# Kernel tuning notes

Measured on AMD Instinct MI355X. Metric: run time of the kernel, lower is better.

Reference implementation:

```python
import math
import jax, jax.numpy as jnp
import numpy as np

N_HEADS = 8
GROUPS = 32
EPS = 1e-5


def setup_inputs() -> dict:
    key = jax.random.key(0)
    ks = jax.random.split(key, 4)
    B, C, H, W = 8, 512, 32, 32
    x = jax.random.normal(ks[0], (B, C, H, W), dtype=jnp.float32)
    gn_scale = jnp.ones((C,), dtype=jnp.float32)
    gn_bias = jnp.zeros((C,), dtype=jnp.float32)
    # small init so softmax logits stay in a sane range (original zero-inits
    # proj_out; we use small random weights so the output is non-trivial)
    qkv_w = jax.random.normal(ks[1], (3 * C, C), dtype=jnp.float32) * 0.02
    qkv_b = jnp.zeros((3 * C,), dtype=jnp.float32)
    proj_w = jax.random.normal(ks[2], (C, C), dtype=jnp.float32) * 0.02
    proj_b = jnp.zeros((C,), dtype=jnp.float32)
    return {"x": x, "gn_scale": gn_scale, "gn_bias": gn_bias,
            "qkv_w": qkv_w, "qkv_b": qkv_b,
            "proj_w": proj_w, "proj_b": proj_b}


def reference(x, gn_scale, gn_bias, qkv_w, qkv_b, proj_w, proj_b):
    b, c, H, W = x.shape
    L = H * W
    xr = x.reshape(b, c, L)

    # GroupNorm32: normalize in fp32 over (channels_per_group, L)
    xf = xr.astype(jnp.float32).reshape(b, GROUPS, -1)
    mu = xf.mean(axis=-1, keepdims=True)
    var = xf.var(axis=-1, keepdims=True)
    xn = ((xf - mu) * jax.lax.rsqrt(var + EPS)).reshape(b, c, L)
    xn = (xn * gn_scale[:, None] + gn_bias[:, None]).astype(x.dtype)

    # 1x1 conv QKV projection: [b, 3C, L]
    qkv = jnp.einsum('oc,bcl->bol', qkv_w, xn) + qkv_b[:, None]

    # QKVAttentionLegacy: split 3C axis as (heads, 3*ch)
    ch = c // N_HEADS
    qkv = qkv.reshape(b * N_HEADS, 3 * ch, L)
    q, k, v = qkv[:, :ch], qkv[:, ch:2 * ch], qkv[:, 2 * ch:]
    scale = 1.0 / math.sqrt(math.sqrt(ch))
    w = jnp.einsum('bct,bcs->bts', q * scale, k * scale)  # [b*h, L, L]
    w = jax.nn.softmax(w.astype(jnp.float32), axis=-1).astype(qkv.dtype)
    a = jnp.einsum('bts,bcs->bct', w, v).reshape(b, c, L)

    # 1x1 conv output projection + residual
    h = jnp.einsum('oc,bcl->bol', proj_w, a) + proj_b[:, None]
    return (xr + h).reshape(b, c, H, W)
```

## Files before the change

kernel.cpp:

```cpp
#include <hip/hip_runtime.h>
#include <hip/hip_bf16.h>

typedef __attribute__((ext_vector_type(8))) short v8s;
typedef __attribute__((ext_vector_type(4))) short v4s;
typedef __attribute__((ext_vector_type(8))) unsigned short u16x8;
typedef __attribute__((ext_vector_type(4))) float v4f;

#define MFMA16(a, b, c) __builtin_amdgcn_mfma_f32_16x16x32_bf16((a), (b), (c), 0, 0, 0)

#if __has_builtin(__builtin_amdgcn_mfma_f32_16x16x16_bf16)
#define MFMA16K16(a, b, c) __builtin_amdgcn_mfma_f32_16x16x16_bf16((a), (b), (c), 0, 0, 0)
#elif __has_builtin(__builtin_amdgcn_mfma_f32_16x16x16bf16_1k)
#define MFMA16K16(a, b, c) __builtin_amdgcn_mfma_f32_16x16x16bf16_1k((a), (b), (c), 0, 0, 0)
#else
static __device__ __forceinline__ v4f mfma16k16_asm(v4s a, v4s b, v4f c) {
  v4f d;
  asm("v_mfma_f32_16x16x16_bf16 %0, %1, %2, %3" : "=v"(d) : "v"(a), "v"(b), "v"(c));
  return d;
}
#define MFMA16K16(a, b, c) mfma16k16_asm((a), (b), (c))
#endif

#define GLL16(g, l)                                                        \
  __builtin_amdgcn_global_load_lds(                                        \
      (const __attribute__((address_space(1))) unsigned int*)(g),          \
      (__attribute__((address_space(3))) unsigned int*)(l), 16, 0, 0)

#if __has_builtin(__builtin_amdgcn_exp2f)
__device__ __forceinline__ float exp2n(float x) { return __builtin_amdgcn_exp2f(x); }
#else
__device__ __forceinline__ float exp2n(float x) {
  float r; asm("v_exp_f32 %0, %1" : "=v"(r) : "v"(x)); return r;
}
#endif

__device__ __forceinline__ unsigned short f2bf(float f) {
  union { float f; unsigned u; } v; v.f = f;
  unsigned r = v.u + 0x7fffu + ((v.u >> 16) & 1u);
  return (unsigned short)(r >> 16);
}
__device__ __forceinline__ unsigned packbf2(float lo, float hi) {
  union { float f; unsigned u; } a, b; a.f = lo; b.f = hi;
  return (a.u >> 16) | (b.u & 0xffff0000u);
}

__global__ __launch_bounds__(256) void cvt_gn_kernel(const float* __restrict__ in0,
                                                     unsigned short* __restrict__ out0,
                                                     const float* __restrict__ in1,
                                                     unsigned short* __restrict__ out1,
                                                     int n0, int n1,
                                                     const float* __restrict__ x,
                                                     float2* __restrict__ stats) {
  if (blockIdx.x < 1024) {
    int i = blockIdx.x * 256 + threadIdx.x;
    const float* in; unsigned short* out;
    if (i < n0) { in = in0; out = out0; }
    else        { i -= n0; if (i >= n1) return; in = in1; out = out1; }
    float4 v = ((const float4*)in)[i];
    ushort4 o;
    o.x = f2bf(v.x); o.y = f2bf(v.y); o.z = f2bf(v.z); o.w = f2bf(v.w);
    ((ushort4*)out)[i] = o;
    return;
  }
  const int bg = blockIdx.x - 1024;
  const float4* xp4 = (const float4*)(x + (size_t)bg * 16 * 1024);
  float s = 0.f, ss = 0.f;
  for (int i = threadIdx.x; i < 4096; i += 256) {
    float4 v = xp4[i];
    s  += (v.x + v.y) + (v.z + v.w);
    ss += (v.x * v.x + v.y * v.y) + (v.z * v.z + v.w * v.w);
  }
  #pragma unroll
  for (int d = 1; d < 64; d <<= 1) { s += __shfl_xor(s, d); ss += __shfl_xor(ss, d); }
  __shared__ float red[2][4];
  const int w = threadIdx.x >> 6;
  if ((threadIdx.x & 63) == 0) { red[0][w] = s; red[1][w] = ss; }
  __syncthreads();
  if (threadIdx.x == 0) {
    s  = red[0][0] + red[0][1] + red[0][2] + red[0][3];
    ss = red[1][0] + red[1][1] + red[1][2] + red[1][3];
    const float mu  = s * (1.f / 16384.f);
    const float var = ss * (1.f / 16384.f) - mu * mu;
    stats[bg] = make_float2(mu, rsqrtf(var + 1e-5f));
  }
}

__global__ __launch_bounds__(256) void gnt_kernel(const float* __restrict__ x,
                                                  const float2* __restrict__ stats,
                                                  const float* __restrict__ gsc,
                                                  const float* __restrict__ gbi,
                                                  unsigned short* __restrict__ xnT) {
  const int b = blockIdx.z, l0 = blockIdx.x * 64, c0 = blockIdx.y * 64;
  const float* sp = x + (size_t)b * 512 * 1024;
  unsigned short* dp = xnT + (size_t)b * 1024 * 512;
  __shared__ unsigned T[64][65];
  const int tid = threadIdx.x;
  const int rr = tid >> 3, c8 = (tid & 7) * 8;
  #pragma unroll
  for (int sw = 0; sw < 2; ++sw) {
    const int c = c0 + sw * 32 + rr;
    const float2 st = stats[b * 32 + (c >> 4)];
    const float sc = gsc[c] * st.y;
    const float bi = gbi[c] - st.x * sc;
    const float4* px = (const float4*)(sp + (size_t)c * 1024 + l0 + c8);
    float4 v0 = px[0], v1 = px[1];
    T[sw * 32 + rr][c8 + 0] = f2bf(v0.x * sc + bi);
    T[sw * 32 + rr][c8 + 1] = f2bf(v0.y * sc + bi);
    T[sw * 32 + rr][c8 + 2] = f2bf(v0.z * sc + bi);
    T[sw * 32 + rr][c8 + 3] = f2bf(v0.w * sc + bi);
    T[sw * 32 + rr][c8 + 4] = f2bf(v1.x * sc + bi);
    T[sw * 32 + rr][c8 + 5] = f2bf(v1.y * sc + bi);
    T[sw * 32 + rr][c8 + 6] = f2bf(v1.z * sc + bi);
    T[sw * 32 + rr][c8 + 7] = f2bf(v1.w * sc + bi);
  }
  __syncthreads();
  #pragma unroll
  for (int sw = 0; sw < 2; ++sw) {
    const int ll = sw * 32 + rr;
    u16x8 o;
    #pragma unroll
    for (int j = 0; j < 8; ++j) o[j] = (unsigned short)T[c8 + j][ll];
    *(u16x8*)(dp + (size_t)(l0 + ll) * 512 + c0 + c8) = o;
  }
}

template <bool QKV, int NT>
__global__ __launch_bounds__(256) void gemm_kernel(
    const unsigned short* __restrict__ A,
    const unsigned short* __restrict__ BT,
    const float* __restrict__ bias,
    const float* __restrict__ xres,
    float* __restrict__ outf,
    unsigned short* __restrict__ qT,
    unsigned short* __restrict__ kT,
    unsigned short* __restrict__ vO) {
  constexpr int K = 512;
  constexpr int NFR = NT / 32;
  constexpr int NJOB = 16 + NT / 8;
  const int n0 = blockIdx.x * NT, m0 = blockIdx.y * 128, b = blockIdx.z;
  const unsigned short* Bp = BT + (size_t)b * 1024 * K;

  __shared__ __align__(16) unsigned short As[128][64];
  __shared__ __align__(16) unsigned short Bs[NT][64];

  const int tid = threadIdx.x, lane = tid & 63, w = tid >> 6;
  const int quad = lane >> 4, l15 = lane & 15;
  const int wm = (w >> 1) * 64, wn = (w & 1) * (NT / 2);
  const int srow = lane >> 3;
  const int scol = ((lane & 7) ^ srow) * 8;
  const int ck0 = ((quad ^ (l15 & 7)) * 8);
  const int ck1 = ck0 ^ 32;
  const unsigned short* Asf = &As[0][0];
  const unsigned short* Bsf = &Bs[0][0];

  v4f acc[4][NFR];
  #pragma unroll
  for (int i = 0; i < 4; ++i)
    #pragma unroll
    for (int j = 0; j < NFR; ++j) acc[i][j] = (v4f){0.f, 0.f, 0.f, 0.f};

  for (int kk = 0; kk < K; kk += 64) {
    __syncthreads();
    #pragma unroll
    for (int jj = 0; jj < NJOB / 4; ++jj) {
      const int job = w * (NJOB / 4) + jj;
      if (job < 16) {
        GLL16(A + (size_t)(m0 + job * 8 + srow) * K + kk + scol, &As[job * 8][0]);
      } else {
        const int j2 = job - 16;
        GLL16(Bp + (size_t)(n0 + j2 * 8 + srow) * K + kk + scol, &Bs[j2 * 8][0]);
      }
    }
    __syncthreads();
    #pragma unroll
    for (int h = 0; h < 2; ++h) {
      const int ck = h ? ck1 : ck0;
      v8s af[4], bf[NFR];
      #pragma unroll
      for (int mt = 0; mt < 4; ++mt) af[mt] = *(const v8s*)(Asf + (wm + mt * 16 + l15) * 64 + ck);
      #pragma unroll
      for (int nt = 0; nt < NFR; ++nt) bf[nt] = *(const v8s*)(Bsf + (wn + nt * 16 + l15) * 64 + ck);
      #pragma unroll
      for (int mt = 0; mt < 4; ++mt)
        #pragma unroll
        for (int nt = 0; nt < NFR; ++nt)
          acc[mt][nt] = MFMA16(af[mt], bf[nt], acc[mt][nt]);
    }
  }

  if (QKV) {
    const int bh8 = b * 8;
    const float cs = 0.18033688011112042f;
    #pragma unroll
    for (int mt = 0; mt < 4; ++mt) {
      const int m4 = m0 + wm + mt * 16 + quad * 4;
      const int h = m4 / 192;
      const int rr = m4 - h * 192;
      const int part = rr >> 6;
      const int ch = rr & 63;
      const float b0 = bias[m4], b1 = bias[m4 + 1], b2 = bias[m4 + 2], b3 = bias[m4 + 3];
      #pragma unroll
      for (int nt = 0; nt < NFR; ++nt) {
        const int n = n0 + wn + nt * 16 + l15;
        v4f a = acc[mt][nt];
        const float v0 = a[0] + b0, v1 = a[1] + b1, v2 = a[2] + b2, v3 = a[3] + b3;
        if (part == 0) {
          ushort4 st4;
          st4.x = f2bf(v0 * cs); st4.y = f2bf(v1 * cs);
          st4.z = f2bf(v2 * cs); st4.w = f2bf(v3 * cs);
          *(ushort4*)(qT + ((size_t)(bh8 + h) * 1024 + n) * 64 + ch) = st4;
        } else if (part == 1) {
          ushort4 st4;
          st4.x = f2bf(v0); st4.y = f2bf(v1); st4.z = f2bf(v2); st4.w = f2bf(v3);
          *(ushort4*)(kT + ((size_t)(bh8 + h) * 1024 + n) * 64 + ch) = st4;
        } else {
          unsigned short* dp = vO + ((size_t)(bh8 + h) * 64 + ch) * 1024 + n;
          dp[0] = f2bf(v0); dp[1024] = f2bf(v1); dp[2048] = f2bf(v2); dp[3072] = f2bf(v3);
        }
      }
    }
  } else {
    #pragma unroll
    for (int mt = 0; mt < 4; ++mt) {
      const int m4 = m0 + wm + mt * 16 + quad * 4;
      const float b0 = bias[m4], b1 = bias[m4 + 1], b2 = bias[m4 + 2], b3 = bias[m4 + 3];
      #pragma unroll
      for (int nt = 0; nt < NFR; ++nt) {
        const int n = n0 + wn + nt * 16 + l15;
        const size_t i0 = ((size_t)b * 512 + m4) * 1024 + n;
        outf[i0]        = xres[i0]        + acc[mt][nt][0] + b0;
        outf[i0 + 1024] = xres[i0 + 1024] + acc[mt][nt][1] + b1;
        outf[i0 + 2048] = xres[i0 + 2048] + acc[mt][nt][2] + b2;
        outf[i0 + 3072] = xres[i0 + 3072] + acc[mt][nt][3] + b3;
      }
    }
  }
}

__global__ __launch_bounds__(256) void attn_kernel(const unsigned short* __restrict__ qT,
                                                   const unsigned short* __restrict__ kT,
                                                   const unsigned short* __restrict__ vv,
                                                   unsigned short* __restrict__ aT) {
  const int bh = blockIdx.x;
  const int t0 = blockIdx.y * 128;
  const unsigned short* qb = qT + (size_t)bh * 1024 * 64;
  const unsigned short* kb = kT + (size_t)bh * 1024 * 64;
  const unsigned short* vb = vv + (size_t)bh * 64 * 1024;

  __shared__ __align__(16) unsigned short Ks[2][128][64];
  __shared__ __align__(16) unsigned short Vs[2][2][64][64];

  const int tid = threadIdx.x, w = tid >> 6, lane = tid & 63;
  const int quad = lane >> 4, l15 = lane & 15;
  const int srow = lane >> 3;
  const int scol = ((lane & 7) ^ srow) * 8;
  const int ck0 = ((quad ^ (l15 & 7)) * 8);
  const int ck1 = ck0 ^ 32;

  #pragma unroll
  for (int jj = 0; jj < 4; ++jj) {
    const int seg = w * 4 + jj;
    GLL16(qb + (size_t)(t0 + seg * 8 + srow) * 64 + scol, &Ks[0][seg * 8][0]);
  }
  __syncthreads();
  v8s qf[2][2];
  #pragma unroll
  for (int tg = 0; tg < 2; ++tg) {
    qf[tg][0] = *(const v8s*)(&Ks[0][0][0] + (w * 32 + tg * 16 + l15) * 64 + ck0);
    qf[tg][1] = *(const v8s*)(&Ks[0][0][0] + (w * 32 + tg * 16 + l15) * 64 + ck1);
  }
  __syncthreads();

  #pragma unroll
  for (int jj = 0; jj < 8; ++jj) {
    const int j = w * 8 + jj;
    if (j < 16) {
      GLL16(kb + (size_t)(j * 8 + srow) * 64 + scol, &Ks[0][j * 8][0]);
    } else {
      const int j2 = j - 16, hf = j2 >> 3, cg = (j2 & 7) * 8;
      GLL16(vb + (size_t)(cg + srow) * 1024 + hf * 64 + scol, &Vs[0][hf][cg][0]);
    }
  }

  v4f o[2][4];
  #pragma unroll
  for (int tg = 0; tg < 2; ++tg)
    #pragma unroll
    for (int i = 0; i < 4; ++i) o[tg][i] = (v4f){0.f, 0.f, 0.f, 0.f};
  float lsum[2] = {0.f, 0.f};

  const int vq4 = (quad & 1) * 4;
  const int vqh = quad >> 1;

  for (int it = 0; it < 8; ++it) {
    __syncthreads();
    if (it + 1 < 8) {
      const int s1 = (it + 1) * 128, bp1 = (it + 1) & 1;
      #pragma unroll
      for (int jj = 0; jj < 8; ++jj) {
        const int j = w * 8 + jj;
        if (j < 16) {
          GLL16(kb + (size_t)(s1 + j * 8 + srow) * 64 + scol, &Ks[bp1][j * 8][0]);
        } else {
          const int j2 = j - 16, hf = j2 >> 3, cg = (j2 & 7) * 8;
          GLL16(vb + (size_t)(cg + srow) * 1024 + s1 + hf * 64 + scol,
                &Vs[bp1][hf][cg][0]);
        }
      }
    }
    const int buf = it & 1;

    #pragma unroll
    for (int hf = 0; hf < 2; ++hf) {
      const unsigned short* Kb = &Ks[buf][hf * 64][0];
      const unsigned short* Vb = &Vs[buf][hf][0][0];

      v4f sa[2][4];
      #pragma unroll
      for (int st = 0; st < 4; ++st) {
        v8s k0 = *(const v8s*)(Kb + (st * 16 + l15) * 64 + ck0);
        v8s k1 = *(const v8s*)(Kb + (st * 16 + l15) * 64 + ck1);
        #pragma unroll
        for (int tg = 0; tg < 2; ++tg) {
          v4f z = (v4f){0.f, 0.f, 0.f, 0.f};
          z = MFMA16(k0, qf[tg][0], z);
          sa[tg][st] = MFMA16(k1, qf[tg][1], z);
        }
      }

      union { v4s v; unsigned u[2]; } pa[2][4];
      #pragma unroll
      for (int tg = 0; tg < 2; ++tg) {
        float rsum = 0.f;
        #pragma unroll
        for (int st = 0; st < 4; ++st) {
          float p0 = exp2n(sa[tg][st][0]);
          float p1 = exp2n(sa[tg][st][1]);
          float p2 = exp2n(sa[tg][st][2]);
          float p3 = exp2n(sa[tg][st][3]);
          rsum += (p0 + p1) + (p2 + p3);
          pa[tg][st].u[0] = packbf2(p0, p1);
          pa[tg][st].u[1] = packbf2(p2, p3);
        }
        lsum[tg] += rsum;
      }

      #pragma unroll
      for (int nc = 0; nc < 4; ++nc) {
        const int row = nc * 16 + l15;
        const unsigned short* vrow = Vb + row * 64 + vq4;
        const int rx = row & 7;
        #pragma unroll
        for (int st = 0; st < 4; ++st) {
          v4s vb4 = *(const v4s*)(vrow + ((st * 2 + vqh) ^ rx) * 8);
          o[0][nc] = MFMA16K16(pa[0][st].v, vb4, o[0][nc]);
          o[1][nc] = MFMA16K16(pa[1][st].v, vb4, o[1][nc]);
        }
      }
    }
  }

  const int b = bh >> 3, h = bh & 7;
  #pragma unroll
  for (int tg = 0; tg < 2; ++tg) {
    lsum[tg] += __shfl_xor(lsum[tg], 16);
    lsum[tg] += __shfl_xor(lsum[tg], 32);
  }
  #pragma unroll
  for (int tg = 0; tg < 2; ++tg) {
    float rl[4];
    #pragma unroll
    for (int r = 0; r < 4; ++r) rl[r] = 1.0f / __shfl(lsum[tg], quad * 4 + r);
    #pragma unroll
    for (int nc = 0; nc < 4; ++nc)
      #pragma unroll
      for (int r = 0; r < 4; ++r) {
        aT[((size_t)b * 1024 + t0 + w * 32 + tg * 16 + quad * 4 + r) * 512 +
           h * 64 + nc * 16 + l15] = f2bf(o[tg][nc][r] * rl[r]);
      }
  }
}

extern "C" void kernel_launch(void* const* d_in, const int* in_sizes, int n_in,
                              void* d_out, int out_size, void* d_ws, size_t ws_size,
                              hipStream_t stream) {
  const float* x    = (const float*)d_in[0];
  const float* gsc  = (const float*)d_in[1];
  const float* gbi  = (const float*)d_in[2];
  const float* qkvw = (const float*)d_in[3];
  const float* qkvb = (const float*)d_in[4];
  const float* pjw  = (const float*)d_in[5];
  const float* pjb  = (const float*)d_in[6];
  float* out = (float*)d_out;

  unsigned short* ws  = (unsigned short*)d_ws;
  unsigned short* qw  = ws;
  unsigned short* pw  = qw + 786432;
  float2* stats = (float2*)(pw + 262144);
  unsigned short* xnT = pw + 262144 + 1024;
  unsigned short* qT  = xnT + 4194304;
  unsigned short* kT  = qT + 4194304;
  unsigned short* vv  = kT + 4194304;
  unsigned short* aT  = vv + 4194304;

  cvt_gn_kernel<<<dim3(1280), dim3(256), 0, stream>>>(qkvw, qw, pjw, pw, 196608, 65536,
                                                      x, stats);
  gnt_kernel<<<dim3(16, 8, 8), dim3(256), 0, stream>>>(x, stats, gsc, gbi, xnT);
  gemm_kernel<true, 128><<<dim3(8, 12, 8), dim3(256), 0, stream>>>(
      qw, xnT, qkvb, nullptr, nullptr, qT, kT, vv);
  attn_kernel<<<dim3(64, 8), dim3(256), 0, stream>>>(qT, kT, vv, aT);
  gemm_kernel<false, 64><<<dim3(16, 4, 8), dim3(256), 0, stream>>>(
      pw, aT, pjb, x, out, nullptr, nullptr, nullptr);
}
```

Before: 149.3 us.

## Double attention query tile per block to reuse K/V fragments across more rows

Each attention block now handles 256 query rows instead of 128, so each wave processes 64 query rows and K/V tiles loaded into LDS are reused across twice as many queries. K and V fragments are hoisted into registers once per half-tile and reused across four query groups, with the score/softmax/PV computation restructured per query group. This halves K/V global and LDS traffic per query but halves the grid to 256 blocks and raises register pressure, which may reduce occupancy. The Q load writes 256 rows into the Ks buffer spanning both double-buffer slots.

```diff
diff --git a/kernel.cpp b/kernel.cpp
--- a/kernel.cpp
+++ b/kernel.cpp
@@ -242,7 +242,7 @@
                                                    const unsigned short* __restrict__ vv,
                                                    unsigned short* __restrict__ aT) {
   const int bh = blockIdx.x;
-  const int t0 = blockIdx.y * 128;
+  const int t0 = blockIdx.y * 256;
   const unsigned short* qb = qT + (size_t)bh * 1024 * 64;
   const unsigned short* kb = kT + (size_t)bh * 1024 * 64;
   const unsigned short* vb = vv + (size_t)bh * 64 * 1024;
@@ -258,16 +258,17 @@
   const int ck1 = ck0 ^ 32;
 
   #pragma unroll
-  for (int jj = 0; jj < 4; ++jj) {
-    const int seg = w * 4 + jj;
-    GLL16(qb + (size_t)(t0 + seg * 8 + srow) * 64 + scol, &Ks[0][seg * 8][0]);
+  for (int jj = 0; jj < 8; ++jj) {
+    const int seg = w * 8 + jj;
+    GLL16(qb + (size_t)(t0 + seg * 8 + srow) * 64 + scol, &Ks[0][0][0] + seg * 8 * 64);
   }
   __syncthreads();
-  v8s qf[2][2];
-  #pragma unroll
-  for (int tg = 0; tg < 2; ++tg) {
-    qf[tg][0] = *(const v8s*)(&Ks[0][0][0] + (w * 32 + tg * 16 + l15) * 64 + ck0);
-    qf[tg][1] = *(const v8s*)(&Ks[0][0][0] + (w * 32 + tg * 16 + l15) * 64 + ck1);
+  v8s qf[4][2];
+  #pragma unroll
+  for (int tg = 0; tg < 4; ++tg) {
+    const int row = w * 64 + tg * 16 + l15;
+    qf[tg][0] = *(const v8s*)(&Ks[0][0][0] + row * 64 + ck0);
+    qf[tg][1] = *(const v8s*)(&Ks[0][0][0] + row * 64 + ck1);
   }
   __syncthreads();
 
@@ -282,12 +283,12 @@
     }
   }
 
-  v4f o[2][4];
-  #pragma unroll
-  for (int tg = 0; tg < 2; ++tg)
+  v4f o[4][4];
+  #pragma unroll
+  for (int tg = 0; tg < 4; ++tg)
     #pragma unroll
     for (int i = 0; i < 4; ++i) o[tg][i] = (v4f){0.f, 0.f, 0.f, 0.f};
-  float lsum[2] = {0.f, 0.f};
+  float lsum[4] = {0.f, 0.f, 0.f, 0.f};
 
   const int vq4 = (quad & 1) * 4;
   const int vqh = quad >> 1;
@@ -315,59 +316,62 @@
       const unsigned short* Kb = &Ks[buf][hf * 64][0];
       const unsigned short* Vb = &Vs[buf][hf][0][0];
 
-      v4f sa[2][4];
+      v8s kf[4][2];
       #pragma unroll
       for (int st = 0; st < 4; ++st) {
-        v8s k0 = *(const v8s*)(Kb + (st * 16 + l15) * 64 + ck0);
-        v8s k1 = *(const v8s*)(Kb + (st * 16 + l15) * 64 + ck1);
-        #pragma unroll
-        for (int tg = 0; tg < 2; ++tg) {
-          v4f z = (v4f){0.f, 0.f, 0.f, 0.f};
-          z = MFMA16(k0, qf[tg][0], z);
-          sa[tg][st] = MFMA16(k1, qf[tg][1], z);
-        }
-      }
-
-      union { v4s v; unsigned u[2]; } pa[2][4];
-      #pragma unroll
-      for (int tg = 0; tg < 2; ++tg) {
-        float rsum = 0.f;
-        #pragma unroll
-        for (int st = 0; st < 4; ++st) {
-          float p0 = exp2n(sa[tg][st][0]);
-          float p1 = exp2n(sa[tg][st][1]);
-          float p2 = exp2n(sa[tg][st][2]);
-          float p3 = exp2n(sa[tg][st][3]);
-          rsum += (p0 + p1) + (p2 + p3);
-          pa[tg][st].u[0] = packbf2(p0, p1);
-          pa[tg][st].u[1] = packbf2(p2, p3);
-        }
-        lsum[tg] += rsum;
-      }
-
+        kf[st][0] = *(const v8s*)(Kb + (st * 16 + l15) * 64 + ck0);
+        kf[st][1] = *(const v8s*)(Kb + (st * 16 + l15) * 64 + ck1);
+      }
+      v4s vfr[4][4];
       #pragma unroll
       for (int nc = 0; nc < 4; ++nc) {
         const int row = nc * 16 + l15;
         const unsigned short* vrow = Vb + row * 64 + vq4;
         const int rx = row & 7;
         #pragma unroll
+        for (int st = 0; st < 4; ++st)
+          vfr[nc][st] = *(const v4s*)(vrow + ((st * 2 + vqh) ^ rx) * 8);
+      }
+
+      #pragma unroll
+      for (int tg = 0; tg < 4; ++tg) {
+        v4f sa[4];
+        #pragma unroll
         for (int st = 0; st < 4; ++st) {
-          v4s vb4 = *(const v4s*)(vrow + ((st * 2 + vqh) ^ rx) * 8);
-          o[0][nc] = MFMA16K16(pa[0][st].v, vb4, o[0][nc]);
-          o[1][nc] = MFMA16K16(pa[1][st].v, vb4, o[1][nc]);
+          v4f z = (v4f){0.f, 0.f, 0.f, 0.f};
+          z = MFMA16(kf[st][0], qf[tg][0], z);
+          sa[st] = MFMA16(kf[st][1], qf[tg][1], z);
         }
+        union { v4s v; unsigned u[2]; } pa[4];
+        float rsum = 0.f;
+        #pragma unroll
+        for (int st = 0; st < 4; ++st) {
+          float p0 = exp2n(sa[st][0]);
+          float p1 = exp2n(sa[st][1]);
+          float p2 = exp2n(sa[st][2]);
+          float p3 = exp2n(sa[st][3]);
+          rsum += (p0 + p1) + (p2 + p3);
+          pa[st].u[0] = packbf2(p0, p1);
+          pa[st].u[1] = packbf2(p2, p3);
+        }
+        lsum[tg] += rsum;
+        #pragma unroll
+        for (int nc = 0; nc < 4; ++nc)
+          #pragma unroll
+          for (int st = 0; st < 4; ++st)
+            o[tg][nc] = MFMA16K16(pa[st].v, vfr[nc][st], o[tg][nc]);
       }
     }
   }
 
   const int b = bh >> 3, h = bh & 7;
   #pragma unroll
-  for (int tg = 0; tg < 2; ++tg) {
+  for (int tg = 0; tg < 4; ++tg) {
     lsum[tg] += __shfl_xor(lsum[tg], 16);
     lsum[tg] += __shfl_xor(lsum[tg], 32);
   }
   #pragma unroll
-  for (int tg = 0; tg < 2; ++tg) {
+  for (int tg = 0; tg < 4; ++tg) {
     float rl[4];
     #pragma unroll
     for (int r = 0; r < 4; ++r) rl[r] = 1.0f / __shfl(lsum[tg], quad * 4 + r);
@@ -375,7 +379,7 @@
     for (int nc = 0; nc < 4; ++nc)
       #pragma unroll
       for (int r = 0; r < 4; ++r) {
-        aT[((size_t)b * 1024 + t0 + w * 32 + tg * 16 + quad * 4 + r) * 512 +
+        aT[((size_t)b * 1024 + t0 + w * 64 + tg * 16 + quad * 4 + r) * 512 +
            h * 64 + nc * 16 + l15] = f2bf(o[tg][nc][r] * rl[r]);
       }
   }
@@ -408,7 +412,7 @@
   gnt_kernel<<<dim3(16, 8, 8), dim3(256), 0, stream>>>(x, stats, gsc, gbi, xnT);
   gemm_kernel<true, 128><<<dim3(8, 12, 8), dim3(256), 0, stream>>>(
       qw, xnT, qkvb, nullptr, nullptr, qT, kT, vv);
-  attn_kernel<<<dim3(64, 8), dim3(256), 0, stream>>>(qT, kT, vv, aT);
+  attn_kernel<<<dim3(64, 4), dim3(256), 0, stream>>>(qT, kT, vv, aT);
   gemm_kernel<false, 64><<<dim3(16, 4, 8), dim3(256), 0, stream>>>(
       pw, aT, pjb, x, out, nullptr, nullptr, nullptr);
 }
```

Measured after the change: 148.0 us. Within noise of the previous version (-0.9%).
